# Performance work log

Measured on AMD Instinct MI355X. Metric: run time of the kernel, lower is better.

Reference implementation:

```python
import jax, jax.numpy as jnp
import numpy as np

D_HEAD = 64


def precompute_rope(d_head, max_seq_len):
    theta = 10000.0 ** (-jnp.arange(0, d_head, 2, dtype=jnp.float32) / d_head)
    positions = jnp.arange(max_seq_len, dtype=jnp.float32)
    angles = jnp.outer(positions, theta)  # [T, d_head/2]
    cos = jnp.repeat(jnp.cos(angles), 2, axis=-1)  # [T, d_head]
    sin = jnp.repeat(jnp.sin(angles), 2, axis=-1)
    return cos, sin


def apply_rope(x, cos, sin):
    # x: [B, H, T, d_head]; cos/sin: [T, d_head] (already sliced to T)
    x_even = x[..., 0::2]
    x_odd = x[..., 1::2]
    x2 = jnp.stack([-x_odd, x_even], axis=-1).reshape(x.shape)  # rotate-half interleaved
    return x * cos + x2 * sin


def setup_inputs() -> dict:
    key = jax.random.key(0)
    k1, k2, k3 = jax.random.split(key, 3)
    B, T, C = 4, 2048, 1024
    x = jax.random.normal(k1, (B, T, C), dtype=jnp.float32)
    mask = jnp.tril(jnp.ones((T, T), dtype=jnp.int32))[None, None]  # causal [1,1,T,T]
    Wqkv = jax.random.normal(k2, (3 * C, C), dtype=jnp.float32) * (1.0 / np.sqrt(C))
    Wout = jax.random.normal(k3, (C, C), dtype=jnp.float32) * (1.0 / np.sqrt(C))
    return {"x": x, "mask": mask, "Wqkv": Wqkv, "Wout": Wout}


def reference(x, mask, Wqkv, Wout):
    B, T, C = x.shape
    n_heads = 16
    d_head = C // n_heads
    cos, sin = precompute_rope(d_head, T)

    qkv = (x @ Wqkv.T).reshape(B, T, 3, n_heads, d_head)
    q, k, v = qkv[:, :, 0], qkv[:, :, 1], qkv[:, :, 2]
    q = jnp.transpose(q, (0, 2, 1, 3))  # [B, H, T, d]
    k = jnp.transpose(k, (0, 2, 1, 3))
    v = jnp.transpose(v, (0, 2, 1, 3))

    q = apply_rope(q, cos, sin)
    k = apply_rope(k, cos, sin)

    attn = jnp.einsum('bhqd,bhkd->bhqk', q, k) / jnp.sqrt(jnp.float32(d_head))
    attn = jnp.where(mask[:, :, :T, :T] == 0, -jnp.inf, attn)
    attn = jax.nn.softmax(attn, axis=-1)

    out = jnp.einsum('bhqk,bhkd->bhqd', attn, v)
    out = jnp.transpose(out, (0, 2, 1, 3)).reshape(B, T, C)
    return out @ Wout.T
```

## Files before the change

### kernel.cpp

```cpp
#include <hip/hip_runtime.h>

typedef unsigned short u16;
typedef unsigned int   u32;
typedef __bf16 bf16;
typedef bf16  bf16x8 __attribute__((ext_vector_type(8)));
typedef u16   u16x8  __attribute__((ext_vector_type(8)));
typedef u32   u32x4  __attribute__((ext_vector_type(4)));
typedef float f32x4  __attribute__((ext_vector_type(4)));
typedef float f32x16 __attribute__((ext_vector_type(16)));

__device__ __forceinline__ u16 f2bf(float f) {
  u32 u = __builtin_bit_cast(u32, f);
  u32 r = u + 0x7fffu + ((u >> 16) & 1u);
  return (u16)(r >> 16);
}

__device__ __forceinline__ u32 cvtpk(float lo, float hi) {
  u32 r;
  asm("v_cvt_pk_bf16_f32 %0, %1, %2" : "=v"(r) : "v"(lo), "v"(hi));
  return r;
}

__device__ __forceinline__ bf16x8 ldb8(const u16* p) {
  return __builtin_bit_cast(bf16x8, *reinterpret_cast<const u16x8*>(p));
}

__device__ __forceinline__ f32x4 mfma16(bf16x8 a, bf16x8 b, f32x4 c) {
  return __builtin_amdgcn_mfma_f32_16x16x32_bf16(a, b, c, 0, 0, 0);
}

__device__ __forceinline__ f32x16 mfma32(bf16x8 a, bf16x8 b, f32x16 c) {
  return __builtin_amdgcn_mfma_f32_32x32x16_bf16(a, b, c, 0, 0, 0);
}

__device__ __forceinline__ void gl_lds16(const void* g, void* l) {
  __builtin_amdgcn_global_load_lds(
      (const __attribute__((address_space(1))) void*)g,
      (__attribute__((address_space(3))) void*)l, 16, 0, 0);
}

__device__ __forceinline__ void stage128x64(const u16* gbase, u16* lds, int tid) {
#pragma unroll
  for (int rd = 0; rd < 4; rd++) {
    int o = rd * 4096 + tid * 16;
    int row = o >> 7, colb = o & 127;
    gl_lds16((const char*)gbase + (size_t)row * 2048 + colb, (char*)lds + o);
  }
}
__device__ __forceinline__ void stage64x64(const u16* gbase, u16* lds, int tid) {
#pragma unroll
  for (int rd = 0; rd < 2; rd++) {
    int o = rd * 4096 + tid * 16;
    int row = o >> 7, colb = o & 127;
    gl_lds16((const char*)gbase + (size_t)row * 2048 + colb, (char*)lds + o);
  }
}

__device__ __forceinline__ void stage_swz(const u16* g, u16* lds, int tid, int rd) {
  int o = rd * 8192 + tid * 16;
  int row = o >> 7;
  int slot = (tid & 7) ^ (row & 7);
  gl_lds16((const char*)g + (size_t)row * 2048 + slot * 16, (char*)lds + o);
}

__device__ __forceinline__ size_t qk_frag_addr(int bh, int t, int d) {
  return (size_t)bh * 131072 + (size_t)(t >> 5) * 2048 +
         (size_t)((d >> 4) * 512 + ((d >> 3) & 1) * 256 + (t & 31) * 8 + (d & 7));
}
__device__ __forceinline__ size_t v_frag_addr(int bh, int t, int d) {
  return (size_t)bh * 131072 + (size_t)(t >> 5) * 2048 +
         (size_t)((d >> 5) * 1024 + ((t >> 4) & 1) * 512 +
                  (((t >> 3) & 1) * 32 + (d & 31)) * 8 + (t & 7));
}

__global__ void cvt_bf16(const float* __restrict__ in, u16* __restrict__ out, int n4) {
  int stride = gridDim.x * blockDim.x;
  for (int i = blockIdx.x * blockDim.x + threadIdx.x; i < n4; i += stride) {
    float4 f = reinterpret_cast<const float4*>(in)[i];
    ushort4 o;
    o.x = f2bf(f.x); o.y = f2bf(f.y); o.z = f2bf(f.z); o.w = f2bf(f.w);
    reinterpret_cast<ushort4*>(out)[i] = o;
  }
}

__global__ void rope_tab(float* __restrict__ ct, float* __restrict__ st) {
  int idx = blockIdx.x * 256 + threadIdx.x;
  int t = idx >> 5, i = idx & 31;
  float theta = exp2f(-(float)i * 0.4152410118609203f);
  float ang = (float)t * theta;
  ct[idx] = cosf(ang);
  st[idx] = sinf(ang);
}

__global__ __launch_bounds__(512) void gemm_qkv(
    const u16* __restrict__ xb, const u16* __restrict__ wb,
    u16* __restrict__ qfb, u16* __restrict__ kfb, u16* __restrict__ vfb,
    const float* __restrict__ cost, const float* __restrict__ sint) {
  __shared__ u16 As[3][256 * 64];
  __shared__ u16 Bs[3][128 * 64];
  int tid = threadIdx.x, lane = tid & 63, wid = tid >> 6;
  int wm = wid >> 1, wn = wid & 1;
  int lr = lane & 15, lk = lane >> 4;
  int m0 = blockIdx.y * 256, n0 = blockIdx.x * 128;
  const u16* gA = xb + (size_t)m0 * 1024;
  const u16* gB = wb + (size_t)n0 * 1024;
  int swz = lr & 7;

  f32x4 acc[4][4] = {};

#pragma unroll
  for (int rd = 0; rd < 4; rd++) stage_swz(gA, As[0], tid, rd);
#pragma unroll
  for (int rd = 0; rd < 2; rd++) stage_swz(gB, Bs[0], tid, rd);
#pragma unroll
  for (int rd = 0; rd < 4; rd++) stage_swz(gA + 64, As[1], tid, rd);
#pragma unroll
  for (int rd = 0; rd < 2; rd++) stage_swz(gB + 64, Bs[1], tid, rd);
  asm volatile("s_waitcnt vmcnt(6)" ::: "memory");
  __builtin_amdgcn_s_barrier();

#pragma unroll 1
  for (int t = 0; t < 16; t++) {
    const u16* Ac = As[t % 3];
    const u16* Bc = Bs[t % 3];
    u16* An = As[(t + 2) % 3];
    u16* Bn = Bs[(t + 2) % 3];
    const u16* gAn = gA + (t + 2) * 64;
    const u16* gBn = gB + (t + 2) * 64;
    bool pf = (t <= 13);
    bf16x8 af[4], bfr[4];

#pragma unroll
    for (int mr = 0; mr < 4; mr++)
      af[mr] = ldb8(&Ac[(wm * 64 + mr * 16 + lr) * 64 + ((lk ^ swz) * 8)]);
#pragma unroll
    for (int nr = 0; nr < 4; nr++)
      bfr[nr] = ldb8(&Bc[(wn * 64 + nr * 16 + lr) * 64 + ((lk ^ swz) * 8)]);
    if (pf) {
      stage_swz(gAn, An, tid, 0);
      stage_swz(gAn, An, tid, 1);
      stage_swz(gBn, Bn, tid, 0);
    }
    __builtin_amdgcn_s_setprio(1);
#pragma unroll
    for (int mr = 0; mr < 4; mr++)
#pragma unroll
      for (int nr = 0; nr < 4; nr++)
        acc[mr][nr] = mfma16(af[mr], bfr[nr], acc[mr][nr]);
    __builtin_amdgcn_s_setprio(0);
    __builtin_amdgcn_s_barrier();

#pragma unroll
    for (int mr = 0; mr < 4; mr++)
      af[mr] = ldb8(&Ac[(wm * 64 + mr * 16 + lr) * 64 + (((lk + 4) ^ swz) * 8)]);
#pragma unroll
    for (int nr = 0; nr < 4; nr++)
      bfr[nr] = ldb8(&Bc[(wn * 64 + nr * 16 + lr) * 64 + (((lk + 4) ^ swz) * 8)]);
    if (pf) {
      stage_swz(gAn, An, tid, 2);
      stage_swz(gAn, An, tid, 3);
      stage_swz(gBn, Bn, tid, 1);
    }
    __builtin_amdgcn_s_setprio(1);
#pragma unroll
    for (int mr = 0; mr < 4; mr++)
#pragma unroll
      for (int nr = 0; nr < 4; nr++)
        acc[mr][nr] = mfma16(af[mr], bfr[nr], acc[mr][nr]);
    __builtin_amdgcn_s_setprio(0);
    if (t < 14) {
      asm volatile("s_waitcnt vmcnt(6)" ::: "memory");
    } else if (t == 14) {
      asm volatile("s_waitcnt vmcnt(0)" ::: "memory");
    }
    __builtin_amdgcn_s_barrier();
  }

  const float CQ = 0.18033688011112042f;
  int sec = n0 >> 10;

  if (sec < 2) {
    u16* buf = (sec == 0) ? qfb : kfb;
    float scale = (sec == 0) ? CQ : 1.0f;
#pragma unroll
    for (int nr = 0; nr < 4; nr++) {
      int col = n0 + wn * 64 + nr * 16 + lr;
      int cc = col & 1023;
      int h = cc >> 6, d = cc & 63;
#pragma unroll
      for (int mr = 0; mr < 4; mr++) {
        int Mb = m0 + wm * 64 + mr * 16 + lk * 4;
#pragma unroll
        for (int r = 0; r < 4; r++) {
          int M = Mb + r;
          int b = M >> 11, tt = M & 2047;
          float val = acc[mr][nr][r];
          float par = __shfl_xor(val, 1);
          float c_ = cost[tt * 32 + (d >> 1)];
          float s_ = sint[tt * 32 + (d >> 1)];
          float res = (d & 1) ? (val * c_ + par * s_) : (val * c_ - par * s_);
          buf[qk_frag_addr(b * 16 + h, tt, d)] = f2bf(res * scale);
        }
      }
    }
  } else {
#pragma unroll
    for (int nr = 0; nr < 4; nr++) {
      int col = n0 + wn * 64 + nr * 16 + lr;
      int cc = col & 1023;
      int h = cc >> 6, d = cc & 63;
#pragma unroll
      for (int mr = 0; mr < 4; mr++) {
        int Mb = m0 + wm * 64 + mr * 16 + lk * 4;
        int b = Mb >> 11, tt = Mb & 2047;
        ushort4 pk;
        pk.x = f2bf(acc[mr][nr][0]); pk.y = f2bf(acc[mr][nr][1]);
        pk.z = f2bf(acc[mr][nr][2]); pk.w = f2bf(acc[mr][nr][3]);
        *reinterpret_cast<ushort4*>(&vfb[v_frag_addr(b * 16 + h, tt, d)]) = pk;
      }
    }
  }
}

__device__ __forceinline__ void attn_step(
    const u16* __restrict__ kfb, const u16* __restrict__ vfb,
    const bf16x8* qf, bf16x8 ones, int kt, int qt, int qrow,
    int lane, int hi,
    f32x16& o0, f32x16& o1, f32x16& lsum, float& m_) {
  const u16* ktb = kfb + (size_t)kt * 2048;
  const u16* vtb = vfb + (size_t)kt * 2048;
  bf16x8 vf00 = ldb8(vtb + lane * 8);
  bf16x8 vf01 = ldb8(vtb + 512 + lane * 8);
  bf16x8 vf10 = ldb8(vtb + 1024 + lane * 8);
  bf16x8 vf11 = ldb8(vtb + 1536 + lane * 8);

  f32x16 sT = {};
#pragma unroll
  for (int s = 0; s < 4; s++) {
    bf16x8 kf = ldb8(ktb + s * 512 + lane * 8);
    sT = mfma32(kf, qf[s], sT);
  }
  if (kt == qt) {
    int k0 = kt * 32;
#pragma unroll
    for (int r = 0; r < 16; r++) {
      int kvg = k0 + (r & 3) + 8 * (r >> 2) + 4 * hi;
      if (kvg > qrow) sT[r] = -3.0e38f;
    }
  }
  float a0 = fmaxf(fmaxf(sT[0], sT[1]),  sT[2]);
  float a1 = fmaxf(fmaxf(sT[3], sT[4]),  sT[5]);
  float a2 = fmaxf(fmaxf(sT[6], sT[7]),  sT[8]);
  float a3 = fmaxf(fmaxf(sT[9], sT[10]), sT[11]);
  float a4 = fmaxf(fmaxf(sT[12], sT[13]), sT[14]);
  float b0 = fmaxf(fmaxf(a0, a1), a2);
  float b1 = fmaxf(fmaxf(a3, a4), sT[15]);
  float pm = fmaxf(b0, b1);
  pm = fmaxf(pm, __shfl_xor(pm, 32));

  if (__any(pm > m_ + 8.0f)) {
    float mn = fmaxf(m_, pm);
    float corr = exp2f(m_ - mn);
    lsum[0] *= corr;
    o0 *= corr; o1 *= corr;
    m_ = mn;
  }

  float p[16];
#pragma unroll
  for (int r = 0; r < 16; r++) p[r] = exp2f(sT[r] - m_);

  u32 c0 = cvtpk(p[0], p[1]),   c1 = cvtpk(p[2], p[3]);
  u32 c2 = cvtpk(p[4], p[5]),   c3 = cvtpk(p[6], p[7]);
  u32 c4 = cvtpk(p[8], p[9]),   c5 = cvtpk(p[10], p[11]);
  u32 c6 = cvtpk(p[12], p[13]), c7 = cvtpk(p[14], p[15]);
  u32 x0 = __shfl_xor((int)c0, 32), x1 = __shfl_xor((int)c1, 32);
  u32 x2 = __shfl_xor((int)c2, 32), x3 = __shfl_xor((int)c3, 32);
  u32 x4 = __shfl_xor((int)c4, 32), x5 = __shfl_xor((int)c5, 32);
  u32 x6 = __shfl_xor((int)c6, 32), x7 = __shfl_xor((int)c7, 32);
  u32x4 w0 = { hi ? x2 : c0, hi ? x3 : c1, hi ? c2 : x0, hi ? c3 : x1 };
  u32x4 w1 = { hi ? x6 : c4, hi ? x7 : c5, hi ? c6 : x4, hi ? c7 : x5 };
  bf16x8 pf0 = __builtin_bit_cast(bf16x8, w0);
  bf16x8 pf1 = __builtin_bit_cast(bf16x8, w1);

  lsum = mfma32(ones, pf0, lsum);
  lsum = mfma32(ones, pf1, lsum);

  o0 = mfma32(vf00, pf0, o0);
  o0 = mfma32(vf01, pf1, o0);
  o1 = mfma32(vf10, pf0, o1);
  o1 = mfma32(vf11, pf1, o1);
}

__device__ __forceinline__ void stash_state(
    float* o_l, float* ml, int lane,
    const f32x16& o0, const f32x16& o1, float m_, float l_) {
#pragma unroll
  for (int r = 0; r < 16; r++) {
    o_l[r * 64 + lane]        = o0[r];
    o_l[(16 + r) * 64 + lane] = o1[r];
  }
  ml[lane]      = m_;
  ml[64 + lane] = l_;
}

__device__ __forceinline__ void merge_state(
    const float* o_l, const float* ml, int lane,
    f32x16& o0, f32x16& o1, float& m_, float& l_) {
  float me = ml[lane], le = ml[64 + lane];
  float mn = fmaxf(m_, me);
  float sc = exp2f(m_ - mn), se = exp2f(me - mn);
  l_ = l_ * sc + le * se;
#pragma unroll
  for (int r = 0; r < 16; r++) {
    o0[r] = o0[r] * sc + o_l[r * 64 + lane] * se;
    o1[r] = o1[r] * sc + o_l[(16 + r) * 64 + lane] * se;
  }
  m_ = mn;
}

__device__ __forceinline__ void attn_half(
    const u16* __restrict__ qfb, const u16* __restrict__ kfb,
    const u16* __restrict__ vfb, u16* __restrict__ og,
    float* o_lds, float* ml_lds, bf16x8 ones,
    int qt, int kt0, int w, int lane, int l31, int hi,
    size_t outbase) {
  int qrow = qt * 32 + l31;
  bf16x8 qf[4];
#pragma unroll
  for (int s = 0; s < 4; s++)
    qf[s] = ldb8(qfb + (size_t)qt * 2048 + s * 512 + lane * 8);

  f32x16 o0 = {}, o1 = {}, lsum = {};
  float m_ = -3.0e38f;

#pragma unroll 1
  for (int kt = kt0; kt <= qt; kt += 4)
    attn_step(kfb, vfb, qf, ones, kt, qt, qrow, lane, hi, o0, o1, lsum, m_);

  float l_ = lsum[0];

  if (w >= 2) stash_state(o_lds + (w - 2) * 2048, ml_lds + (w - 2) * 128, lane, o0, o1, m_, l_);
  __syncthreads();
  if (w < 2)  merge_state(o_lds + w * 2048, ml_lds + w * 128, lane, o0, o1, m_, l_);
  __syncthreads();
  if (w == 1) stash_state(o_lds, ml_lds, lane, o0, o1, m_, l_);
  __syncthreads();
  if (w == 0) {
    merge_state(o_lds, ml_lds, lane, o0, o1, m_, l_);
    float inv = 1.0f / l_;
    size_t base = outbase + (size_t)qrow * 1024;
#pragma unroll
    for (int db = 0; db < 2; db++) {
      f32x16 oo = db ? o1 : o0;
#pragma unroll
      for (int r = 0; r < 16; r += 2) {
        int d = db * 32 + (r & 3) + 8 * (r >> 2) + 4 * hi;
        u32 pk_ = cvtpk(oo[r] * inv, oo[r + 1] * inv);
        *reinterpret_cast<u32*>(&og[base + d]) = pk_;
      }
    }
  }
  __syncthreads();
}

__global__ __launch_bounds__(256, 4) void attn_fwd(
    const u16* __restrict__ qg, const u16* __restrict__ kg,
    const u16* __restrict__ vg, u16* __restrict__ og) {
  __shared__ float o_lds[2 * 32 * 64];
  __shared__ float ml_lds[2 * 2 * 64];
  int tid = threadIdx.x, lane = tid & 63, w = tid >> 6;
  int l31 = lane & 31, hi = lane >> 5;
  int blk = blockIdx.x;
  int bh = blk & 63, i = blk >> 6;
  const u16* qfb = qg + (size_t)bh * 131072;
  const u16* kfb = kg + (size_t)bh * 131072;
  const u16* vfb = vg + (size_t)bh * 131072;
  int hh = bh & 15, b = bh >> 4;
  size_t outbase = (size_t)b * 2048 * 1024 + hh * 64;

  u16x8 ov = {0x3F80, 0x3F80, 0x3F80, 0x3F80, 0x3F80, 0x3F80, 0x3F80, 0x3F80};
  bf16x8 ones = __builtin_bit_cast(bf16x8, ov);

  attn_half(qfb, kfb, vfb, og, o_lds, ml_lds, ones, i, w, w, lane, l31, hi, outbase);
  attn_half(qfb, kfb, vfb, og, o_lds, ml_lds, ones, 63 - i, (w - i - 1) & 3, w, lane, l31, hi, outbase);
}

__global__ __launch_bounds__(256) void gemm_out(
    const u16* __restrict__ ab, const u16* __restrict__ wb, float* __restrict__ out) {
  __shared__ u16 As[128 * 64];
  __shared__ u16 Bs[64 * 64];
  int tid = threadIdx.x, lane = tid & 63, w = tid >> 6;
  int wm = w >> 1, wn = w & 1;
  int lr = lane & 15, lk = lane >> 4;
  int m0 = blockIdx.y * 128, n0 = blockIdx.x * 64;

  f32x4 acc[4][2] = {};

  for (int k0 = 0; k0 < 1024; k0 += 64) {
    stage128x64(ab + (size_t)m0 * 1024 + k0, As, tid);
    stage64x64(wb + (size_t)n0 * 1024 + k0, Bs, tid);
    asm volatile("s_waitcnt vmcnt(0)" ::: "memory");
    __syncthreads();
#pragma unroll
    for (int kk = 0; kk < 2; kk++) {
      bf16x8 af[4], bfr[2];
#pragma unroll
      for (int mt = 0; mt < 4; mt++) af[mt]  = ldb8(&As[(64 * wm + 16 * mt + lr) * 64 + lk * 8 + 32 * kk]);
#pragma unroll
      for (int nt = 0; nt < 2; nt++) bfr[nt] = ldb8(&Bs[(32 * wn + 16 * nt + lr) * 64 + lk * 8 + 32 * kk]);
#pragma unroll
      for (int mt = 0; mt < 4; mt++)
#pragma unroll
        for (int nt = 0; nt < 2; nt++)
          acc[mt][nt] = mfma16(af[mt], bfr[nt], acc[mt][nt]);
    }
    __syncthreads();
  }

#pragma unroll
  for (int nt = 0; nt < 2; nt++) {
    int col = n0 + 32 * wn + 16 * nt + lr;
#pragma unroll
    for (int mt = 0; mt < 4; mt++) {
      int Mb = m0 + 64 * wm + 16 * mt + lk * 4;
#pragma unroll
      for (int r = 0; r < 4; r++) {
        out[(size_t)(Mb + r) * 1024 + col] = acc[mt][nt][r];
      }
    }
  }
}

extern "C" void kernel_launch(void* const* d_in, const int* in_sizes, int n_in,
                              void* d_out, int out_size, void* d_ws, size_t ws_size,
                              hipStream_t stream) {
  const float* x    = (const float*)d_in[0];
  const float* Wqkv = (const float*)d_in[2];
  const float* Wout = (const float*)d_in[3];
  float* out = (float*)d_out;
  char* ws = (char*)d_ws;

  u16* x_bf    = (u16*)(ws + 0);
  u16* wqkv_bf = (u16*)(ws + 16777216);
  u16* wout_bf = (u16*)(ws + 23068672);
  u16* qf_buf  = (u16*)(ws + 25165824);
  u16* kf_buf  = (u16*)(ws + 41943040);
  u16* vf_buf  = (u16*)(ws + 58720256);
  u16* a_out   = (u16*)(ws + 75497472);
  float* cost  = (float*)(ws + 92274688);
  float* sint  = (float*)(ws + 92536832);

  cvt_bf16<<<2048, 256, 0, stream>>>(x, x_bf, 8388608 / 4);
  cvt_bf16<<<768, 256, 0, stream>>>(Wqkv, wqkv_bf, 3145728 / 4);
  cvt_bf16<<<256, 256, 0, stream>>>(Wout, wout_bf, 1048576 / 4);
  rope_tab<<<256, 256, 0, stream>>>(cost, sint);
  gemm_qkv<<<dim3(24, 32), 512, 0, stream>>>(x_bf, wqkv_bf, qf_buf, kf_buf, vf_buf, cost, sint);
  attn_fwd<<<2048, 256, 0, stream>>>(qf_buf, kf_buf, vf_buf, a_out);
  gemm_out<<<dim3(16, 64), 256, 0, stream>>>(a_out, wout_bf, out);
}
```

Measured before the change: 186.2 us.

## Rewrite output projection GEMM with larger tiles, triple-buffered swizzled LDS pipeline

The output projection GEMM moves from 128x64 tiles with 256 threads and a synchronous load-wait-compute loop to 256x128 tiles with 512 threads. LDS is triple-buffered, and global-to-LDS prefetch runs two k-steps ahead, interleaved with the MFMA phases using partial vmcnt waits. An XOR swizzle reduces LDS bank conflicts, and s_setprio raises MFMA priority. The goal is to hide global load latency and raise data reuse per block. The grid drops to 256 blocks and LDS use rises sharply, which may reduce occupancy or leave CUs idle.

```diff
diff --git a/kernel.cpp b/kernel.cpp
--- a/kernel.cpp
+++ b/kernel.cpp
@@ -37,23 +37,6 @@
   __builtin_amdgcn_global_load_lds(
       (const __attribute__((address_space(1))) void*)g,
       (__attribute__((address_space(3))) void*)l, 16, 0, 0);
-}
-
-__device__ __forceinline__ void stage128x64(const u16* gbase, u16* lds, int tid) {
-#pragma unroll
-  for (int rd = 0; rd < 4; rd++) {
-    int o = rd * 4096 + tid * 16;
-    int row = o >> 7, colb = o & 127;
-    gl_lds16((const char*)gbase + (size_t)row * 2048 + colb, (char*)lds + o);
-  }
-}
-__device__ __forceinline__ void stage64x64(const u16* gbase, u16* lds, int tid) {
-#pragma unroll
-  for (int rd = 0; rd < 2; rd++) {
-    int o = rd * 4096 + tid * 16;
-    int row = o >> 7, colb = o & 127;
-    gl_lds16((const char*)gbase + (size_t)row * 2048 + colb, (char*)lds + o);
-  }
 }
 
 __device__ __forceinline__ void stage_swz(const u16* g, u16* lds, int tid, int rd) {
@@ -386,47 +369,97 @@
   attn_half(qfb, kfb, vfb, og, o_lds, ml_lds, ones, 63 - i, (w - i - 1) & 3, w, lane, l31, hi, outbase);
 }
 
-__global__ __launch_bounds__(256) void gemm_out(
+__global__ __launch_bounds__(512) void gemm_out(
     const u16* __restrict__ ab, const u16* __restrict__ wb, float* __restrict__ out) {
-  __shared__ u16 As[128 * 64];
-  __shared__ u16 Bs[64 * 64];
-  int tid = threadIdx.x, lane = tid & 63, w = tid >> 6;
-  int wm = w >> 1, wn = w & 1;
+  __shared__ u16 As[3][256 * 64];
+  __shared__ u16 Bs[3][128 * 64];
+  int tid = threadIdx.x, lane = tid & 63, wid = tid >> 6;
+  int wm = wid >> 1, wn = wid & 1;
   int lr = lane & 15, lk = lane >> 4;
-  int m0 = blockIdx.y * 128, n0 = blockIdx.x * 64;
-
-  f32x4 acc[4][2] = {};
-
-  for (int k0 = 0; k0 < 1024; k0 += 64) {
-    stage128x64(ab + (size_t)m0 * 1024 + k0, As, tid);
-    stage64x64(wb + (size_t)n0 * 1024 + k0, Bs, tid);
-    asm volatile("s_waitcnt vmcnt(0)" ::: "memory");
-    __syncthreads();
-#pragma unroll
-    for (int kk = 0; kk < 2; kk++) {
-      bf16x8 af[4], bfr[2];
-#pragma unroll
-      for (int mt = 0; mt < 4; mt++) af[mt]  = ldb8(&As[(64 * wm + 16 * mt + lr) * 64 + lk * 8 + 32 * kk]);
-#pragma unroll
-      for (int nt = 0; nt < 2; nt++) bfr[nt] = ldb8(&Bs[(32 * wn + 16 * nt + lr) * 64 + lk * 8 + 32 * kk]);
-#pragma unroll
-      for (int mt = 0; mt < 4; mt++)
-#pragma unroll
-        for (int nt = 0; nt < 2; nt++)
-          acc[mt][nt] = mfma16(af[mt], bfr[nt], acc[mt][nt]);
-    }
-    __syncthreads();
-  }
-
-#pragma unroll
-  for (int nt = 0; nt < 2; nt++) {
-    int col = n0 + 32 * wn + 16 * nt + lr;
-#pragma unroll
-    for (int mt = 0; mt < 4; mt++) {
-      int Mb = m0 + 64 * wm + 16 * mt + lk * 4;
+  int m0 = blockIdx.y * 256, n0 = blockIdx.x * 128;
+  const u16* gA = ab + (size_t)m0 * 1024;
+  const u16* gB = wb + (size_t)n0 * 1024;
+  int swz = lr & 7;
+
+  f32x4 acc[4][4] = {};
+
+#pragma unroll
+  for (int rd = 0; rd < 4; rd++) stage_swz(gA, As[0], tid, rd);
+#pragma unroll
+  for (int rd = 0; rd < 2; rd++) stage_swz(gB, Bs[0], tid, rd);
+#pragma unroll
+  for (int rd = 0; rd < 4; rd++) stage_swz(gA + 64, As[1], tid, rd);
+#pragma unroll
+  for (int rd = 0; rd < 2; rd++) stage_swz(gB + 64, Bs[1], tid, rd);
+  asm volatile("s_waitcnt vmcnt(6)" ::: "memory");
+  __builtin_amdgcn_s_barrier();
+
+#pragma unroll 1
+  for (int t = 0; t < 16; t++) {
+    const u16* Ac = As[t % 3];
+    const u16* Bc = Bs[t % 3];
+    u16* An = As[(t + 2) % 3];
+    u16* Bn = Bs[(t + 2) % 3];
+    const u16* gAn = gA + (t + 2) * 64;
+    const u16* gBn = gB + (t + 2) * 64;
+    bool pf = (t <= 13);
+    bf16x8 af[4], bfr[4];
+
+#pragma unroll
+    for (int mr = 0; mr < 4; mr++)
+      af[mr] = ldb8(&Ac[(wm * 64 + mr * 16 + lr) * 64 + ((lk ^ swz) * 8)]);
+#pragma unroll
+    for (int nr = 0; nr < 4; nr++)
+      bfr[nr] = ldb8(&Bc[(wn * 64 + nr * 16 + lr) * 64 + ((lk ^ swz) * 8)]);
+    if (pf) {
+      stage_swz(gAn, An, tid, 0);
+      stage_swz(gAn, An, tid, 1);
+      stage_swz(gBn, Bn, tid, 0);
+    }
+    __builtin_amdgcn_s_setprio(1);
+#pragma unroll
+    for (int mr = 0; mr < 4; mr++)
+#pragma unroll
+      for (int nr = 0; nr < 4; nr++)
+        acc[mr][nr] = mfma16(af[mr], bfr[nr], acc[mr][nr]);
+    __builtin_amdgcn_s_setprio(0);
+    __builtin_amdgcn_s_barrier();
+
+#pragma unroll
+    for (int mr = 0; mr < 4; mr++)
+      af[mr] = ldb8(&Ac[(wm * 64 + mr * 16 + lr) * 64 + (((lk + 4) ^ swz) * 8)]);
+#pragma unroll
+    for (int nr = 0; nr < 4; nr++)
+      bfr[nr] = ldb8(&Bc[(wn * 64 + nr * 16 + lr) * 64 + (((lk + 4) ^ swz) * 8)]);
+    if (pf) {
+      stage_swz(gAn, An, tid, 2);
+      stage_swz(gAn, An, tid, 3);
+      stage_swz(gBn, Bn, tid, 1);
+    }
+    __builtin_amdgcn_s_setprio(1);
+#pragma unroll
+    for (int mr = 0; mr < 4; mr++)
+#pragma unroll
+      for (int nr = 0; nr < 4; nr++)
+        acc[mr][nr] = mfma16(af[mr], bfr[nr], acc[mr][nr]);
+    __builtin_amdgcn_s_setprio(0);
+    if (t < 14) {
+      asm volatile("s_waitcnt vmcnt(6)" ::: "memory");
+    } else if (t == 14) {
+      asm volatile("s_waitcnt vmcnt(0)" ::: "memory");
+    }
+    __builtin_amdgcn_s_barrier();
+  }
+
+#pragma unroll
+  for (int nr = 0; nr < 4; nr++) {
+    int col = n0 + wn * 64 + nr * 16 + lr;
+#pragma unroll
+    for (int mr = 0; mr < 4; mr++) {
+      int Mb = m0 + wm * 64 + mr * 16 + lk * 4;
 #pragma unroll
       for (int r = 0; r < 4; r++) {
-        out[(size_t)(Mb + r) * 1024 + col] = acc[mt][nt][r];
+        out[(size_t)(Mb + r) * 1024 + col] = acc[mr][nr][r];
       }
     }
   }
@@ -457,5 +490,5 @@
   rope_tab<<<256, 256, 0, stream>>>(cost, sint);
   gemm_qkv<<<dim3(24, 32), 512, 0, stream>>>(x_bf, wqkv_bf, qf_buf, kf_buf, vf_buf, cost, sint);
   attn_fwd<<<2048, 256, 0, stream>>>(qf_buf, kf_buf, vf_buf, a_out);
-  gemm_out<<<dim3(16, 64), 256, 0, stream>>>(a_out, wout_bf, out);
-}
+  gemm_out<<<dim3(8, 32), 512, 0, stream>>>(a_out, wout_bf, out);
+}
```

After: 179.4 us. 3.7% less time.
